# Kernel tuning notes

Hardware: AMD Instinct MI355X
Metric: run time of the kernel (lower is better)

The kernel has to match this reference:

```python
import jax, jax.numpy as jnp
import numpy as np

TEMPERATURE = 0.1
INF = 1e8
SIGMA = (5.0, 1.0)
LABEL_TYPE = ("cont", "cat")
CAT_SIM = (0.0, 0.5)
ALPHA = (1.0, 1.0)
N, D = 4096, 128


def _label_weights(y, label_type, sigma, cat_sim):
    # y: [2N] label values; returns row-normalized RBF weight matrix [2N, 2N]
    gamma = 1.0 / (2.0 * sigma ** 2)
    d2 = (y[:, None] - y[None, :]) ** 2
    w = jnp.exp(-gamma * d2)
    if label_type == "cat":
        # rbf == 1 exactly iff labels equal; others snapped to cat_similarity
        w = jnp.where(w == 1.0, 1.0, cat_sim)
    n2 = w.shape[0]
    w = w * (1.0 - jnp.eye(n2, dtype=w.dtype))
    w = w / jnp.sum(w, axis=1, keepdims=True)
    return w


def setup_inputs() -> dict:
    key = jax.random.key(0)
    k1, k2, k3, k4 = jax.random.split(key, 4)
    z_i = jax.random.normal(k1, (N, D), dtype=jnp.float32)
    z_j = jax.random.normal(k2, (N, D), dtype=jnp.float32)
    cont = jax.random.normal(k3, (N,), dtype=jnp.float32) * 10.0  # e.g. age
    cat = jax.random.randint(k4, (N,), 0, 3).astype(jnp.float32)   # e.g. class id
    labels = jnp.stack([cont, cat], axis=1)  # [N, 2]
    return {"z_i": z_i, "z_j": z_j, "labels": labels}


def reference(z_i, z_j, labels):
    n = z_i.shape[0]
    zi = z_i / jnp.linalg.norm(z_i, axis=-1, keepdims=True)
    zj = z_j / jnp.linalg.norm(z_j, axis=-1, keepdims=True)
    eye = INF * jnp.eye(n, dtype=zi.dtype)
    sim_zii = zi @ zi.T / TEMPERATURE - eye
    sim_zjj = zj @ zj.T / TEMPERATURE - eye
    sim_zij = zi @ zj.T / TEMPERATURE
    sim_Z = jnp.concatenate(
        [jnp.concatenate([sim_zii, sim_zij], axis=1),
         jnp.concatenate([sim_zij.T, sim_zjj], axis=1)], axis=0)  # [2N, 2N]
    log_sim_Z = jax.nn.log_softmax(sim_Z, axis=1)
    loss = jnp.zeros((), dtype=sim_Z.dtype)
    for i, (lt, s, cs, a) in enumerate(zip(LABEL_TYPE, SIGMA, CAT_SIM, ALPHA)):
        y = jnp.tile(labels[:, i], 2)  # [2N] == repeat(2,1).flatten()
        w = _label_weights(y, lt, s, cs)
        loss = loss + (-1.0 / n) * jnp.sum(w * log_sim_Z) * a
    return loss
```

## Files before the change

### kernel.cpp

```cpp
#include <hip/hip_runtime.h>
#include <hip/hip_bf16.h>
#include <math.h>

#define NP 4096
#define DD 128
#define N2 8192
#define TINV 10.0f
#define SHIFT 10.0f
#define C1 14.4269504f
#define NGL2 -0.0288539004f

typedef __attribute__((ext_vector_type(8))) short bf16x8;
typedef __attribute__((ext_vector_type(4))) float f32x4;
typedef __attribute__((ext_vector_type(4))) int i32x4;

__device__ __forceinline__ float bf2f(short s) {
  return __uint_as_float(((unsigned)(unsigned short)s) << 16);
}

#define GLDS(g, l)                                                                   \
  __builtin_amdgcn_global_load_lds((__attribute__((address_space(1))) const void*)(g), \
                                   (__attribute__((address_space(3))) void*)(l), 16, 0, 0)

__device__ __forceinline__ float dpp_red16(float x) {
  x += __int_as_float(__builtin_amdgcn_update_dpp(0, __float_as_int(x), 0x101, 0xF, 0xF, true));
  x += __int_as_float(__builtin_amdgcn_update_dpp(0, __float_as_int(x), 0x102, 0xF, 0xF, true));
  x += __int_as_float(__builtin_amdgcn_update_dpp(0, __float_as_int(x), 0x104, 0xF, 0xF, true));
  x += __int_as_float(__builtin_amdgcn_update_dpp(0, __float_as_int(x), 0x108, 0xF, 0xF, true));
  return x;
}

__global__ __launch_bounds__(256) void kprep(const float* __restrict__ zi,
                                             const float* __restrict__ zj,
                                             const float* __restrict__ labels,
                                             __hip_bfloat16* __restrict__ Z,
                                             float4* __restrict__ rowinfo,
                                             double* __restrict__ accd,
                                             unsigned int* __restrict__ cnt,
                                             float* __restrict__ zsc) {
  int w = threadIdx.x >> 6, lane = threadIdx.x & 63;
  if (blockIdx.x < 2048) {
    int a = blockIdx.x * 4 + w;
    const float* src = (a < NP) ? (zi + (size_t)a * DD) : (zj + (size_t)(a - NP) * DD);
    float2 v = *(const float2*)(src + lane * 2);
    float ss = v.x * v.x + v.y * v.y;
#pragma unroll
    for (int m = 1; m < 64; m <<= 1) ss += __shfl_xor(ss, m);
    float rn = rsqrtf(ss);
    __hip_bfloat162 o;
    o.x = __float2bfloat16(v.x * rn);
    o.y = __float2bfloat16(v.y * rn);
    *(__hip_bfloat162*)(Z + (size_t)a * DD + lane * 2) = o;
  } else {
    int a = blockIdx.x - 2048;
    if (a == 0) {
      if (threadIdx.x == 0) { *accd = 0.0; *cnt = 0u; }
      for (int q = threadIdx.x; q < 384; q += 256) zsc[q] = 0.f;
    }
    float ca = labels[a * 2 + 0], ga = labels[a * 2 + 1];
    float s1 = 0.f, c2 = 0.f;
    for (int m = threadIdx.x; m < NP; m += 256) {
      float2 lm = *(const float2*)(labels + m * 2);
      float dy = ca - lm.x;
      s1 += __builtin_amdgcn_exp2f(dy * dy * NGL2);
      c2 += (ga == lm.y) ? 1.f : 0.f;
    }
#pragma unroll
    for (int m = 1; m < 64; m <<= 1) {
      s1 += __shfl_xor(s1, m);
      c2 += __shfl_xor(c2, m);
    }
    __shared__ float sh[8];
    if (lane == 0) { sh[w] = s1; sh[4 + w] = c2; }
    __syncthreads();
    if (threadIdx.x == 0) {
      s1 = sh[0] + sh[1] + sh[2] + sh[3];
      c2 = sh[4] + sh[5] + sh[6] + sh[7];
      float rs1 = 2.f * s1 - 1.f;
      float rs2 = (float)NP + c2 - 1.f;
      float4 ri = make_float4(ca, TINV / rs1, ga, TINV / rs2);
      rowinfo[a] = ri;
      rowinfo[a + NP] = ri;
    }
  }
}

__global__ __launch_bounds__(512, 4) void kmain(const __hip_bfloat16* __restrict__ Zp,
                                                const float4* __restrict__ rowinfo,
                                                const float* __restrict__ labels,
                                                float2* __restrict__ part,
                                                float* __restrict__ zsc) {
  __shared__ char lds[2 * 128 * 256];

  int id = (blockIdx.x & 7) * 268 + (blockIdx.x >> 3);
  const int t = threadIdx.x;
  const int lane = t & 63, w = t >> 6;

  if (id >= 2080) {
    int b = id - 2080;
    int c = t & 127, rgrp = t >> 7;
    int r0 = b * 128 + rgrp * 32;
    float s0 = 0.f, s1 = 0.f, s2 = 0.f;
    for (int k = 0; k < 32; ++k) {
      int r = r0 + k;
      float zf = bf2f(((const short*)Zp)[(size_t)r * DD + c]);
      float g = labels[(r & (NP - 1)) * 2 + 1];
      s0 += (g == 0.f) ? zf : 0.f;
      s1 += (g == 1.f) ? zf : 0.f;
      s2 += (g == 2.f) ? zf : 0.f;
    }
    float* sh = (float*)lds;
    sh[(rgrp * 3 + 0) * 128 + c] = s0;
    sh[(rgrp * 3 + 1) * 128 + c] = s1;
    sh[(rgrp * 3 + 2) * 128 + c] = s2;
    __syncthreads();
    if (t < 384) {
      int cls = t >> 7, cc = t & 127;
      float v = sh[(0 * 3 + cls) * 128 + cc] + sh[(1 * 3 + cls) * 128 + cc] +
                sh[(2 * 3 + cls) * 128 + cc] + sh[(3 * 3 + cls) * 128 + cc];
      atomicAdd(&zsc[cls * 128 + cc], v);
    }
    return;
  }

  char* ldsA = lds;
  char* ldsB = lds + 128 * 256;
  int tb = id;
  int I = (int)((129.0f - sqrtf(16641.0f - 8.0f * (float)tb)) * 0.5f);
  while (I * (129 - I) / 2 > tb) --I;
  while ((I + 1) * (128 - I) / 2 <= tb) ++I;
  int J = I + (tb - I * (129 - I) / 2);
  const bool diag = (I == J);
  const int row0 = I * 128, col0 = J * 128;
  const char* gZ = (const char*)Zp;
  const char* ldsBp = diag ? ldsA : ldsB;

  const int wr = w >> 2, wc = w & 3;
  const int lrow = lane & 15, lgrp = lane >> 4;

#pragma unroll
  for (int i = 0; i < 4; ++i) {
    int chunk = t + i * 512;
    int r = chunk >> 4;
    int bc = (chunk & 15) << 4;
    int srcc = bc ^ ((r & 7) << 4);
    int uoff = ((t & ~63) + i * 512) * 16;
    GLDS(gZ + (size_t)(row0 + r) * 256 + srcc, ldsA + uoff);
  }
  if (!diag) {
#pragma unroll
    for (int i = 0; i < 4; ++i) {
      int chunk = t + i * 512;
      int r = chunk >> 4;
      int bc = (chunk & 15) << 4;
      int srcc = bc ^ ((r & 7) << 4);
      int uoff = ((t & ~63) + i * 512) * 16;
      GLDS(gZ + (size_t)(col0 + r) * 256 + srcc, ldsB + uoff);
    }
  }
  __syncthreads();

  f32x4 acc[4][2] = {};
#pragma unroll
  for (int kk = 0; kk < 4; ++kk) {
    int bcol = kk * 64 + (lgrp << 4);
    bf16x8 af[4], bfv[2];
#pragma unroll
    for (int mi = 0; mi < 4; ++mi) {
      int r = wr * 64 + mi * 16 + lrow;
      af[mi] = *(const bf16x8*)(ldsA + r * 256 + (bcol ^ ((r & 7) << 4)));
    }
#pragma unroll
    for (int ni = 0; ni < 2; ++ni) {
      int r = wc * 32 + ni * 16 + lrow;
      bfv[ni] = *(const bf16x8*)(ldsBp + r * 256 + (bcol ^ ((r & 7) << 4)));
    }
#pragma unroll
    for (int mi = 0; mi < 4; ++mi)
#pragma unroll
      for (int ni = 0; ni < 2; ++ni)
        acc[mi][ni] = __builtin_amdgcn_mfma_f32_16x16x32_bf16(af[mi], bfv[ni], acc[mi][ni], 0, 0, 0);
  }

  float2 rbv[2];
#pragma unroll
  for (int ni = 0; ni < 2; ++ni)
    rbv[ni] = *(const float2*)&rowinfo[col0 + wc * 32 + ni * 16 + lrow];

  __syncthreads();
  float* lacc = (float*)lds;
  lacc[t] = 0.f;
  __syncthreads();

  if (!diag) {
    float ec[2] = {0.f, 0.f}, pc[2] = {0.f, 0.f};
#pragma unroll
    for (int mi = 0; mi < 4; ++mi) {
      int a0 = row0 + wr * 64 + mi * 16 + lgrp * 4;
#pragma unroll
      for (int j = 0; j < 4; ++j) {
        float2 ri = *(const float2*)&rowinfo[a0 + j];
        float es = 0.f, pa = 0.f;
#pragma unroll
        for (int ni = 0; ni < 2; ++ni) {
          float v = acc[mi][ni][j];
          float e = __builtin_amdgcn_exp2f(fmaf(v, C1, -C1));
          float dy = ri.x - rbv[ni].x;
          float wu = __builtin_amdgcn_exp2f(dy * dy * NGL2);
          es += e;
          ec[ni] += e;
          pa = fmaf(wu, v, pa);
          pc[ni] = fmaf(wu, v, pc[ni]);
        }
        es = dpp_red16(es);
        float wsum = dpp_red16(pa * ri.y);
        if (lrow == 0) {
          int idx = wr * 64 + mi * 16 + lgrp * 4 + j;
          atomicAdd(&lacc[2 * idx], es);
          atomicAdd(&lacc[2 * idx + 1], wsum);
        }
      }
    }
#pragma unroll
    for (int ni = 0; ni < 2; ++ni) {
      float wcol = pc[ni] * rbv[ni].y;
      float e2 = ec[ni] + __shfl_xor(ec[ni], 16);
      e2 += __shfl_xor(e2, 32);
      float w2 = wcol + __shfl_xor(wcol, 16);
      w2 += __shfl_xor(w2, 32);
      if (lane < 16) {
        int idx = 128 + wc * 32 + ni * 16 + lane;
        atomicAdd(&lacc[2 * idx], e2);
        atomicAdd(&lacc[2 * idx + 1], w2);
      }
    }
  } else {
#pragma unroll
    for (int mi = 0; mi < 4; ++mi) {
      int a0 = row0 + wr * 64 + mi * 16 + lgrp * 4;
#pragma unroll
      for (int j = 0; j < 4; ++j) {
        int a = a0 + j;
        float2 ri = *(const float2*)&rowinfo[a0 + j];
        float es = 0.f, pa = 0.f;
#pragma unroll
        for (int ni = 0; ni < 2; ++ni) {
          float v = acc[mi][ni][j];
          float nd = (a != col0 + wc * 32 + ni * 16 + lrow) ? 1.f : 0.f;
          float e = __builtin_amdgcn_exp2f(fmaf(v, C1, -C1)) * nd;
          float dy = ri.x - rbv[ni].x;
          float wu = __builtin_amdgcn_exp2f(dy * dy * NGL2) * nd;
          es += e;
          pa = fmaf(wu, v, pa);
        }
        es = dpp_red16(es);
        float wsum = dpp_red16(pa * ri.y);
        if (lrow == 0) {
          int idx = wr * 64 + mi * 16 + lgrp * 4 + j;
          atomicAdd(&lacc[2 * idx], es);
          atomicAdd(&lacc[2 * idx + 1], wsum);
        }
      }
    }
  }

  __syncthreads();
  if (t < 256) ((float2*)part)[(size_t)tb * 256 + t] = ((float2*)lacc)[t];
}

__global__ __launch_bounds__(512) void kreduce(const float2* __restrict__ part,
                                               const __hip_bfloat16* __restrict__ Z,
                                               const float4* __restrict__ rowinfo,
                                               const float* __restrict__ zsc,
                                               double* __restrict__ accd,
                                               unsigned int* __restrict__ cnt,
                                               float* __restrict__ out) {
  int T = blockIdx.x;
  int t = threadIdx.x;
  int r = t & 127, q = t >> 7;
  float es = 0.f, ws = 0.f;
  int tb0 = T * (129 - T) / 2;
  for (int k = q; k < 64 - T; k += 4) {
    float2 v = part[(size_t)(tb0 + k) * 256 + r];
    es += v.x;
    ws += v.y;
  }
  for (int I = q; I < T; I += 4) {
    float2 v = part[(size_t)(I * (129 - I) / 2 + T - I) * 256 + 128 + r];
    es += v.x;
    ws += v.y;
  }
  __shared__ float sess[512], swss[512];
  sess[q * 128 + r] = es;
  swss[q * 128 + r] = ws;
  __syncthreads();

  double val = 0.0;
  if (t < 128) {
    es = sess[t] + sess[128 + t] + sess[256 + t] + sess[384 + t];
    ws = swss[t] + swss[128 + t] + swss[256 + t] + swss[384 + t];
    int a = T * 128 + t;
    float4 ri = rowinfo[a];
    int cls = (int)ri.z;
    const float* zc = zsc + cls * DD;
    float d1 = 0.f, d2 = 0.f;
    const __hip_bfloat16* zrow = Z + (size_t)a * DD;
#pragma unroll
    for (int k = 0; k < 16; ++k) {
      bf16x8 zv = *(const bf16x8*)(zrow + k * 8);
#pragma unroll
      for (int e = 0; e < 8; ++e) {
        int col = k * 8 + e;
        float zf = bf2f(zv[e]);
        float tot = zsc[col] + zsc[128 + col] + zsc[256 + col];
        d1 = fmaf(zf, tot, d1);
        d2 = fmaf(zf, zc[col], d2);
      }
    }
    ws += (0.5f * (d1 - 1.0f) + 0.5f * (d2 - 1.0f)) * ri.w;
    val = (double)ws - 2.0 * (double)(SHIFT + __logf(es));
  }
#pragma unroll
  for (int m = 1; m < 64; m <<= 1) val += __shfl_xor(val, m);
  __shared__ double shd[8];
  if ((t & 63) == 0) shd[t >> 6] = val;
  __syncthreads();
  if (t == 0) {
    double bsum = shd[0] + shd[1] + shd[2] + shd[3] + shd[4] + shd[5] + shd[6] + shd[7];
    atomicAdd(accd, bsum);
    __threadfence();
    unsigned int old = atomicAdd(cnt, 1u);
    if (old == 63u) {
      double tot = atomicAdd(accd, 0.0);
      out[0] = (float)(-tot / (double)NP);
    }
  }
}

extern "C" void kernel_launch(void* const* d_in, const int* in_sizes, int n_in,
                              void* d_out, int out_size, void* d_ws, size_t ws_size,
                              hipStream_t stream) {
  const float* zi = (const float*)d_in[0];
  const float* zj = (const float*)d_in[1];
  const float* labels = (const float*)d_in[2];
  float* out = (float*)d_out;
  char* ws = (char*)d_ws;

  float4* rowinfo = (float4*)ws;
  double* accd = (double*)(ws + 128 * 1024);
  unsigned int* cnt = (unsigned int*)(ws + 128 * 1024 + 8);
  float* zsc = (float*)(ws + 132 * 1024);
  __hip_bfloat16* Z = (__hip_bfloat16*)(ws + 256 * 1024);
  float2* part = (float2*)(ws + 256 * 1024 + 2 * 1024 * 1024);

  kprep<<<6144, 256, 0, stream>>>(zi, zj, labels, Z, rowinfo, accd, cnt, zsc);
  kmain<<<2144, 512, 0, stream>>>(Z, rowinfo, labels, part, zsc);
  kreduce<<<64, 512, 0, stream>>>(part, Z, rowinfo, zsc, accd, cnt, out);
}
```

Baseline: 64.21 us.

## Fuse reduction kernel into main kernel via last-blocks ticket and spin-wait

Removes the separate kreduce launch. Each kmain block takes a ticket from a global atomic counter after writing its partials. The last 64 ticket holders spin until every block has finished, then do the per-row-block reduction and the final accumulation. Partials are now written with atomicExch so they are visible across blocks. This saves one kernel launch and its gap, but the spinning blocks hold CUs and the approach depends on all blocks reaching the counter.

```diff
diff --git a/kernel.cpp b/kernel.cpp
--- a/kernel.cpp
+++ b/kernel.cpp
@@ -9,6 +9,7 @@
 #define SHIFT 10.0f
 #define C1 14.4269504f
 #define NGL2 -0.0288539004f
+#define NBLK 2144
 
 typedef __attribute__((ext_vector_type(8))) short bf16x8;
 typedef __attribute__((ext_vector_type(4))) float f32x4;
@@ -54,7 +55,7 @@
   } else {
     int a = blockIdx.x - 2048;
     if (a == 0) {
-      if (threadIdx.x == 0) { *accd = 0.0; *cnt = 0u; }
+      if (threadIdx.x == 0) { *accd = 0.0; cnt[0] = 0u; cnt[1] = 0u; }
       for (int q = threadIdx.x; q < 384; q += 256) zsc[q] = 0.f;
     }
     float ca = labels[a * 2 + 0], ga = labels[a * 2 + 1];
@@ -89,7 +90,10 @@
                                                 const float4* __restrict__ rowinfo,
                                                 const float* __restrict__ labels,
                                                 float2* __restrict__ part,
-                                                float* __restrict__ zsc) {
+                                                float* __restrict__ zsc,
+                                                double* __restrict__ accd,
+                                                unsigned int* __restrict__ cnt,
+                                                float* __restrict__ out) {
   __shared__ char lds[2 * 128 * 256];
 
   int id = (blockIdx.x & 7) * 268 + (blockIdx.x >> 3);
@@ -120,34 +124,22 @@
                 sh[(2 * 3 + cls) * 128 + cc] + sh[(3 * 3 + cls) * 128 + cc];
       atomicAdd(&zsc[cls * 128 + cc], v);
     }
-    return;
-  }
-
-  char* ldsA = lds;
-  char* ldsB = lds + 128 * 256;
-  int tb = id;
-  int I = (int)((129.0f - sqrtf(16641.0f - 8.0f * (float)tb)) * 0.5f);
-  while (I * (129 - I) / 2 > tb) --I;
-  while ((I + 1) * (128 - I) / 2 <= tb) ++I;
-  int J = I + (tb - I * (129 - I) / 2);
-  const bool diag = (I == J);
-  const int row0 = I * 128, col0 = J * 128;
-  const char* gZ = (const char*)Zp;
-  const char* ldsBp = diag ? ldsA : ldsB;
-
-  const int wr = w >> 2, wc = w & 3;
-  const int lrow = lane & 15, lgrp = lane >> 4;
-
-#pragma unroll
-  for (int i = 0; i < 4; ++i) {
-    int chunk = t + i * 512;
-    int r = chunk >> 4;
-    int bc = (chunk & 15) << 4;
-    int srcc = bc ^ ((r & 7) << 4);
-    int uoff = ((t & ~63) + i * 512) * 16;
-    GLDS(gZ + (size_t)(row0 + r) * 256 + srcc, ldsA + uoff);
-  }
-  if (!diag) {
+  } else {
+    char* ldsA = lds;
+    char* ldsB = lds + 128 * 256;
+    int tb = id;
+    int I = (int)((129.0f - sqrtf(16641.0f - 8.0f * (float)tb)) * 0.5f);
+    while (I * (129 - I) / 2 > tb) --I;
+    while ((I + 1) * (128 - I) / 2 <= tb) ++I;
+    int J = I + (tb - I * (129 - I) / 2);
+    const bool diag = (I == J);
+    const int row0 = I * 128, col0 = J * 128;
+    const char* gZ = (const char*)Zp;
+    const char* ldsBp = diag ? ldsA : ldsB;
+
+    const int wr = w >> 2, wc = w & 3;
+    const int lrow = lane & 15, lgrp = lane >> 4;
+
 #pragma unroll
     for (int i = 0; i < 4; ++i) {
       int chunk = t + i * 512;
@@ -155,184 +147,209 @@
       int bc = (chunk & 15) << 4;
       int srcc = bc ^ ((r & 7) << 4);
       int uoff = ((t & ~63) + i * 512) * 16;
-      GLDS(gZ + (size_t)(col0 + r) * 256 + srcc, ldsB + uoff);
-    }
-  }
-  __syncthreads();
-
-  f32x4 acc[4][2] = {};
-#pragma unroll
-  for (int kk = 0; kk < 4; ++kk) {
-    int bcol = kk * 64 + (lgrp << 4);
-    bf16x8 af[4], bfv[2];
-#pragma unroll
-    for (int mi = 0; mi < 4; ++mi) {
-      int r = wr * 64 + mi * 16 + lrow;
-      af[mi] = *(const bf16x8*)(ldsA + r * 256 + (bcol ^ ((r & 7) << 4)));
-    }
-#pragma unroll
-    for (int ni = 0; ni < 2; ++ni) {
-      int r = wc * 32 + ni * 16 + lrow;
-      bfv[ni] = *(const bf16x8*)(ldsBp + r * 256 + (bcol ^ ((r & 7) << 4)));
-    }
-#pragma unroll
-    for (int mi = 0; mi < 4; ++mi)
-#pragma unroll
-      for (int ni = 0; ni < 2; ++ni)
-        acc[mi][ni] = __builtin_amdgcn_mfma_f32_16x16x32_bf16(af[mi], bfv[ni], acc[mi][ni], 0, 0, 0);
-  }
-
-  float2 rbv[2];
-#pragma unroll
-  for (int ni = 0; ni < 2; ++ni)
-    rbv[ni] = *(const float2*)&rowinfo[col0 + wc * 32 + ni * 16 + lrow];
-
-  __syncthreads();
-  float* lacc = (float*)lds;
-  lacc[t] = 0.f;
-  __syncthreads();
-
-  if (!diag) {
-    float ec[2] = {0.f, 0.f}, pc[2] = {0.f, 0.f};
-#pragma unroll
-    for (int mi = 0; mi < 4; ++mi) {
-      int a0 = row0 + wr * 64 + mi * 16 + lgrp * 4;
-#pragma unroll
-      for (int j = 0; j < 4; ++j) {
-        float2 ri = *(const float2*)&rowinfo[a0 + j];
-        float es = 0.f, pa = 0.f;
-#pragma unroll
-        for (int ni = 0; ni < 2; ++ni) {
-          float v = acc[mi][ni][j];
-          float e = __builtin_amdgcn_exp2f(fmaf(v, C1, -C1));
-          float dy = ri.x - rbv[ni].x;
-          float wu = __builtin_amdgcn_exp2f(dy * dy * NGL2);
-          es += e;
-          ec[ni] += e;
-          pa = fmaf(wu, v, pa);
-          pc[ni] = fmaf(wu, v, pc[ni]);
+      GLDS(gZ + (size_t)(row0 + r) * 256 + srcc, ldsA + uoff);
+    }
+    if (!diag) {
+#pragma unroll
+      for (int i = 0; i < 4; ++i) {
+        int chunk = t + i * 512;
+        int r = chunk >> 4;
+        int bc = (chunk & 15) << 4;
+        int srcc = bc ^ ((r & 7) << 4);
+        int uoff = ((t & ~63) + i * 512) * 16;
+        GLDS(gZ + (size_t)(col0 + r) * 256 + srcc, ldsB + uoff);
+      }
+    }
+    __syncthreads();
+
+    f32x4 acc[4][2] = {};
+#pragma unroll
+    for (int kk = 0; kk < 4; ++kk) {
+      int bcol = kk * 64 + (lgrp << 4);
+      bf16x8 af[4], bfv[2];
+#pragma unroll
+      for (int mi = 0; mi < 4; ++mi) {
+        int r = wr * 64 + mi * 16 + lrow;
+        af[mi] = *(const bf16x8*)(ldsA + r * 256 + (bcol ^ ((r & 7) << 4)));
+      }
+#pragma unroll
+      for (int ni = 0; ni < 2; ++ni) {
+        int r = wc * 32 + ni * 16 + lrow;
+        bfv[ni] = *(const bf16x8*)(ldsBp + r * 256 + (bcol ^ ((r & 7) << 4)));
+      }
+#pragma unroll
+      for (int mi = 0; mi < 4; ++mi)
+#pragma unroll
+        for (int ni = 0; ni < 2; ++ni)
+          acc[mi][ni] = __builtin_amdgcn_mfma_f32_16x16x32_bf16(af[mi], bfv[ni], acc[mi][ni], 0, 0, 0);
+    }
+
+    float2 rbv[2];
+#pragma unroll
+    for (int ni = 0; ni < 2; ++ni)
+      rbv[ni] = *(const float2*)&rowinfo[col0 + wc * 32 + ni * 16 + lrow];
+
+    __syncthreads();
+    float* lacc = (float*)lds;
+    lacc[t] = 0.f;
+    __syncthreads();
+
+    if (!diag) {
+      float ec[2] = {0.f, 0.f}, pc[2] = {0.f, 0.f};
+#pragma unroll
+      for (int mi = 0; mi < 4; ++mi) {
+        int a0 = row0 + wr * 64 + mi * 16 + lgrp * 4;
+#pragma unroll
+        for (int j = 0; j < 4; ++j) {
+          float2 ri = *(const float2*)&rowinfo[a0 + j];
+          float es = 0.f, pa = 0.f;
+#pragma unroll
+          for (int ni = 0; ni < 2; ++ni) {
+            float v = acc[mi][ni][j];
+            float e = __builtin_amdgcn_exp2f(fmaf(v, C1, -C1));
+            float dy = ri.x - rbv[ni].x;
+            float wu = __builtin_amdgcn_exp2f(dy * dy * NGL2);
+            es += e;
+            ec[ni] += e;
+            pa = fmaf(wu, v, pa);
+            pc[ni] = fmaf(wu, v, pc[ni]);
+          }
+          es = dpp_red16(es);
+          float wsum = dpp_red16(pa * ri.y);
+          if (lrow == 0) {
+            int idx = wr * 64 + mi * 16 + lgrp * 4 + j;
+            atomicAdd(&lacc[2 * idx], es);
+            atomicAdd(&lacc[2 * idx + 1], wsum);
+          }
         }
-        es = dpp_red16(es);
-        float wsum = dpp_red16(pa * ri.y);
-        if (lrow == 0) {
-          int idx = wr * 64 + mi * 16 + lgrp * 4 + j;
-          atomicAdd(&lacc[2 * idx], es);
-          atomicAdd(&lacc[2 * idx + 1], wsum);
+      }
+#pragma unroll
+      for (int ni = 0; ni < 2; ++ni) {
+        float wcol = pc[ni] * rbv[ni].y;
+        float e2 = ec[ni] + __shfl_xor(ec[ni], 16);
+        e2 += __shfl_xor(e2, 32);
+        float w2 = wcol + __shfl_xor(wcol, 16);
+        w2 += __shfl_xor(w2, 32);
+        if (lane < 16) {
+          int idx = 128 + wc * 32 + ni * 16 + lane;
+          atomicAdd(&lacc[2 * idx], e2);
+          atomicAdd(&lacc[2 * idx + 1], w2);
         }
       }
-    }
-#pragma unroll
-    for (int ni = 0; ni < 2; ++ni) {
-      float wcol = pc[ni] * rbv[ni].y;
-      float e2 = ec[ni] + __shfl_xor(ec[ni], 16);
-      e2 += __shfl_xor(e2, 32);
-      float w2 = wcol + __shfl_xor(wcol, 16);
-      w2 += __shfl_xor(w2, 32);
-      if (lane < 16) {
-        int idx = 128 + wc * 32 + ni * 16 + lane;
-        atomicAdd(&lacc[2 * idx], e2);
-        atomicAdd(&lacc[2 * idx + 1], w2);
-      }
-    }
-  } else {
-#pragma unroll
-    for (int mi = 0; mi < 4; ++mi) {
-      int a0 = row0 + wr * 64 + mi * 16 + lgrp * 4;
-#pragma unroll
-      for (int j = 0; j < 4; ++j) {
-        int a = a0 + j;
-        float2 ri = *(const float2*)&rowinfo[a0 + j];
-        float es = 0.f, pa = 0.f;
-#pragma unroll
-        for (int ni = 0; ni < 2; ++ni) {
-          float v = acc[mi][ni][j];
-          float nd = (a != col0 + wc * 32 + ni * 16 + lrow) ? 1.f : 0.f;
-          float e = __builtin_amdgcn_exp2f(fmaf(v, C1, -C1)) * nd;
-          float dy = ri.x - rbv[ni].x;
-          float wu = __builtin_amdgcn_exp2f(dy * dy * NGL2) * nd;
-          es += e;
-          pa = fmaf(wu, v, pa);
+    } else {
+#pragma unroll
+      for (int mi = 0; mi < 4; ++mi) {
+        int a0 = row0 + wr * 64 + mi * 16 + lgrp * 4;
+#pragma unroll
+        for (int j = 0; j < 4; ++j) {
+          int a = a0 + j;
+          float2 ri = *(const float2*)&rowinfo[a0 + j];
+          float es = 0.f, pa = 0.f;
+#pragma unroll
+          for (int ni = 0; ni < 2; ++ni) {
+            float v = acc[mi][ni][j];
+            float nd = (a != col0 + wc * 32 + ni * 16 + lrow) ? 1.f : 0.f;
+            float e = __builtin_amdgcn_exp2f(fmaf(v, C1, -C1)) * nd;
+            float dy = ri.x - rbv[ni].x;
+            float wu = __builtin_amdgcn_exp2f(dy * dy * NGL2) * nd;
+            es += e;
+            pa = fmaf(wu, v, pa);
+          }
+          es = dpp_red16(es);
+          float wsum = dpp_red16(pa * ri.y);
+          if (lrow == 0) {
+            int idx = wr * 64 + mi * 16 + lgrp * 4 + j;
+            atomicAdd(&lacc[2 * idx], es);
+            atomicAdd(&lacc[2 * idx + 1], wsum);
+          }
         }
-        es = dpp_red16(es);
-        float wsum = dpp_red16(pa * ri.y);
-        if (lrow == 0) {
-          int idx = wr * 64 + mi * 16 + lgrp * 4 + j;
-          atomicAdd(&lacc[2 * idx], es);
-          atomicAdd(&lacc[2 * idx + 1], wsum);
-        }
-      }
-    }
-  }
-
-  __syncthreads();
-  if (t < 256) ((float2*)part)[(size_t)tb * 256 + t] = ((float2*)lacc)[t];
-}
-
-__global__ __launch_bounds__(512) void kreduce(const float2* __restrict__ part,
-                                               const __hip_bfloat16* __restrict__ Z,
-                                               const float4* __restrict__ rowinfo,
-                                               const float* __restrict__ zsc,
-                                               double* __restrict__ accd,
-                                               unsigned int* __restrict__ cnt,
-                                               float* __restrict__ out) {
-  int T = blockIdx.x;
-  int t = threadIdx.x;
-  int r = t & 127, q = t >> 7;
-  float es = 0.f, ws = 0.f;
-  int tb0 = T * (129 - T) / 2;
-  for (int k = q; k < 64 - T; k += 4) {
-    float2 v = part[(size_t)(tb0 + k) * 256 + r];
-    es += v.x;
-    ws += v.y;
-  }
-  for (int I = q; I < T; I += 4) {
-    float2 v = part[(size_t)(I * (129 - I) / 2 + T - I) * 256 + 128 + r];
-    es += v.x;
-    ws += v.y;
-  }
-  __shared__ float sess[512], swss[512];
-  sess[q * 128 + r] = es;
-  swss[q * 128 + r] = ws;
-  __syncthreads();
-
-  double val = 0.0;
-  if (t < 128) {
-    es = sess[t] + sess[128 + t] + sess[256 + t] + sess[384 + t];
-    ws = swss[t] + swss[128 + t] + swss[256 + t] + swss[384 + t];
-    int a = T * 128 + t;
-    float4 ri = rowinfo[a];
-    int cls = (int)ri.z;
-    const float* zc = zsc + cls * DD;
-    float d1 = 0.f, d2 = 0.f;
-    const __hip_bfloat16* zrow = Z + (size_t)a * DD;
-#pragma unroll
-    for (int k = 0; k < 16; ++k) {
-      bf16x8 zv = *(const bf16x8*)(zrow + k * 8);
-#pragma unroll
-      for (int e = 0; e < 8; ++e) {
-        int col = k * 8 + e;
-        float zf = bf2f(zv[e]);
-        float tot = zsc[col] + zsc[128 + col] + zsc[256 + col];
-        d1 = fmaf(zf, tot, d1);
-        d2 = fmaf(zf, zc[col], d2);
-      }
-    }
-    ws += (0.5f * (d1 - 1.0f) + 0.5f * (d2 - 1.0f)) * ri.w;
-    val = (double)ws - 2.0 * (double)(SHIFT + __logf(es));
-  }
-#pragma unroll
-  for (int m = 1; m < 64; m <<= 1) val += __shfl_xor(val, m);
-  __shared__ double shd[8];
-  if ((t & 63) == 0) shd[t >> 6] = val;
+      }
+    }
+
+    __syncthreads();
+    if (t < 256) {
+      union { float2 f; unsigned long long u; } cv;
+      cv.f = ((float2*)lacc)[t];
+      atomicExch((unsigned long long*)&part[(size_t)tb * 256 + t], cv.u);
+    }
+  }
+
+  __shared__ unsigned int stick;
   __syncthreads();
   if (t == 0) {
-    double bsum = shd[0] + shd[1] + shd[2] + shd[3] + shd[4] + shd[5] + shd[6] + shd[7];
-    atomicAdd(accd, bsum);
     __threadfence();
-    unsigned int old = atomicAdd(cnt, 1u);
-    if (old == 63u) {
-      double tot = atomicAdd(accd, 0.0);
-      out[0] = (float)(-tot / (double)NP);
+    stick = atomicAdd(&cnt[0], 1u);
+  }
+  __syncthreads();
+  unsigned int ticket = stick;
+  if (ticket < NBLK - 64) return;
+  int T = (int)(ticket - (NBLK - 64));
+
+  if (t == 0) {
+    while (atomicAdd(&cnt[0], 0u) < (unsigned)NBLK) __builtin_amdgcn_s_sleep(8);
+  }
+  __syncthreads();
+  __threadfence();
+
+  {
+    int r = t & 127, q = t >> 7;
+    float es = 0.f, ws = 0.f;
+    int tb0 = T * (129 - T) / 2;
+    for (int k = q; k < 64 - T; k += 4) {
+      float2 v = part[(size_t)(tb0 + k) * 256 + r];
+      es += v.x;
+      ws += v.y;
+    }
+    for (int I2 = q; I2 < T; I2 += 4) {
+      float2 v = part[(size_t)(I2 * (129 - I2) / 2 + T - I2) * 256 + 128 + r];
+      es += v.x;
+      ws += v.y;
+    }
+    float* sess = (float*)lds;
+    float* swss = sess + 512;
+    sess[q * 128 + r] = es;
+    swss[q * 128 + r] = ws;
+    __syncthreads();
+
+    double val = 0.0;
+    if (t < 128) {
+      es = sess[t] + sess[128 + t] + sess[256 + t] + sess[384 + t];
+      ws = swss[t] + swss[128 + t] + swss[256 + t] + swss[384 + t];
+      int a = T * 128 + t;
+      float4 ri = rowinfo[a];
+      int cls = (int)ri.z;
+      const float* zc = zsc + cls * DD;
+      float d1 = 0.f, d2 = 0.f;
+      const __hip_bfloat16* zrow = Zp + (size_t)a * DD;
+#pragma unroll
+      for (int k = 0; k < 16; ++k) {
+        bf16x8 zv = *(const bf16x8*)(zrow + k * 8);
+#pragma unroll
+        for (int e = 0; e < 8; ++e) {
+          int col = k * 8 + e;
+          float zf = bf2f(zv[e]);
+          float tot = zsc[col] + zsc[128 + col] + zsc[256 + col];
+          d1 = fmaf(zf, tot, d1);
+          d2 = fmaf(zf, zc[col], d2);
+        }
+      }
+      ws += (0.5f * (d1 - 1.0f) + 0.5f * (d2 - 1.0f)) * ri.w;
+      val = (double)ws - 2.0 * (double)(SHIFT + __logf(es));
+    }
+#pragma unroll
+    for (int m = 1; m < 64; m <<= 1) val += __shfl_xor(val, m);
+    double* shd = (double*)(lds + 4096);
+    if ((t & 63) == 0) shd[t >> 6] = val;
+    __syncthreads();
+    if (t == 0) {
+      double bsum = shd[0] + shd[1] + shd[2] + shd[3] + shd[4] + shd[5] + shd[6] + shd[7];
+      atomicAdd(accd, bsum);
+      __threadfence();
+      unsigned int old2 = atomicAdd(&cnt[1], 1u);
+      if (old2 == 63u) {
+        double tot = atomicAdd(accd, 0.0);
+        out[0] = (float)(-tot / (double)NP);
+      }
     }
   }
 }
@@ -354,6 +371,5 @@
   float2* part = (float2*)(ws + 256 * 1024 + 2 * 1024 * 1024);
 
   kprep<<<6144, 256, 0, stream>>>(zi, zj, labels, Z, rowinfo, accd, cnt, zsc);
-  kmain<<<2144, 512, 0, stream>>>(Z, rowinfo, labels, part, zsc);
-  kreduce<<<64, 512, 0, stream>>>(part, Z, rowinfo, zsc, accd, cnt, out);
-}
+  kmain<<<NBLK, 512, 0, stream>>>(Z, rowinfo, labels, part, zsc, accd, cnt, out);
+}
```

Measured after the change: 102.1 us. 1.59x slower.
